# Kernel optimization log

Measured on AMD Instinct MI355X. Metric: run time of the kernel, lower is better.

## Reference

```python
import jax, jax.numpy as jnp
import numpy as np

B, C_IN, C_OUT, M, K1, K2 = 8, 256, 256, 4096, 4, 4


def _cheb_assemble(K, L, x):
    # x: (B, C_in, M) -> X: (B, C_in, M, K) with X[..., k] = L^k x
    # Batched as a single (M, M) @ (M, B*C_in) GEMM per power step.
    Bv, Cv, Mv = x.shape
    x0 = x.reshape(Bv * Cv, Mv).T  # (M, B*C_in)

    def step(carry, _):
        return L @ carry, carry  # emit L^k x, carry becomes L^{k+1} x

    _, ys = jax.lax.scan(step, x0, None, length=K)  # (K, M, B*C_in)
    return ys.transpose(2, 1, 0).reshape(Bv, Cv, Mv, K)


def setup_inputs() -> dict:
    key = jax.random.key(0)
    k1, k2, k3, k4 = jax.random.split(key, 4)
    scale = 1.0 / np.sqrt(M)  # keep spectral radius O(1) so L^k stays finite
    Ll = jax.random.normal(k1, (M, M), dtype=jnp.float32) * scale
    Lu = jax.random.normal(k2, (M, M), dtype=jnp.float32) * scale
    x = jax.random.normal(k3, (B, C_IN, M), dtype=jnp.float32)
    theta1 = jax.random.normal(k4, (C_OUT, C_IN, K1 + K2), dtype=jnp.float32)  # variance=1.0
    bias1 = jnp.zeros((1, C_OUT, 1), dtype=jnp.float32)
    return {"Ll": Ll, "Lu": Lu, "x": x, "theta1": theta1, "bias1": bias1}


def reference(Ll, Lu, x, theta1, bias1):
    X1 = _cheb_assemble(K1, Ll, x)  # (B, C_in, M, K1)
    X2 = _cheb_assemble(K2, Lu, x)  # (B, C_in, M, K2)
    X = jnp.concatenate((X1, X2), axis=3)  # (B, C_in, M, K1+K2)
    y = jnp.einsum("bimk,oik->bom", X, theta1)
    return y + bias1  # (B, C_out, M)
```

## Files before the change

kernel.cpp:

```cpp
#include <hip/hip_runtime.h>
#include <hip/hip_bf16.h>

typedef __hip_bfloat16 bf16;
typedef __attribute__((ext_vector_type(8))) short bshort8;
typedef __attribute__((ext_vector_type(4))) float f32x4;

#define GLL16(gsrc, ldst)                                                      \
  __builtin_amdgcn_global_load_lds(                                            \
      (const __attribute__((address_space(1))) void*)(gsrc),                   \
      (__attribute__((address_space(3))) void*)(ldst), 16, 0, 0)

#define MEMFENCE asm volatile("" ::: "memory")
#define BARRIER                                                                \
  do {                                                                         \
    MEMFENCE;                                                                  \
    __builtin_amdgcn_s_barrier();                                              \
    MEMFENCE;                                                                  \
  } while (0)
#define WAIT_LGKM0 asm volatile("s_waitcnt lgkmcnt(0)" ::: "memory")
#define WAIT_VM4 asm volatile("s_waitcnt vmcnt(4)" ::: "memory")

__global__ __launch_bounds__(256) void cast_f32_bf16(const float* __restrict__ src,
                                                     bf16* __restrict__ dst, int n4) {
  int stride = gridDim.x * blockDim.x;
  const float4* s4 = reinterpret_cast<const float4*>(src);
  __hip_bfloat162* d2 = reinterpret_cast<__hip_bfloat162*>(dst);
  for (int i = blockIdx.x * blockDim.x + threadIdx.x; i < n4; i += stride) {
    float4 v = s4[i];
    d2[2 * i]     = __float22bfloat162_rn(make_float2(v.x, v.y));
    d2[2 * i + 1] = __float22bfloat162_rn(make_float2(v.z, v.w));
  }
}

__global__ __launch_bounds__(256) void transpose_cast_x(const float* __restrict__ x,
                                                        bf16* __restrict__ Xt) {
  __shared__ bf16 t[64][65];
  int b = blockIdx.z;
  int m0 = blockIdx.x * 64;
  int i0 = blockIdx.y * 64;
  int tx = threadIdx.x & 63;
  int ty = threadIdx.x >> 6;
  for (int ii = ty; ii < 64; ii += 4)
    t[ii][tx] = __float2bfloat16(x[(size_t)(b * 256 + i0 + ii) * 4096 + m0 + tx]);
  __syncthreads();
  for (int mm = ty; mm < 64; mm += 4)
    Xt[(size_t)(b * 4096 + m0 + mm) * 256 + i0 + tx] = t[tx][mm];
}

__global__ __launch_bounds__(256) void build_theta(const float* __restrict__ th,
                                                   bf16* __restrict__ Tall) {
  int idx = blockIdx.x * 256 + threadIdx.x;
  int s = idx >> 16;
  int oi = idx & 65535;
  float v;
  if (s == 0)      v = th[oi * 8 + 0] + th[oi * 8 + 4];
  else if (s <= 3) v = th[oi * 8 + s];
  else             v = th[oi * 8 + s + 1];
  Tall[idx] = __float2bfloat16(v);
}

template <int EPI>
__device__ __forceinline__ void gemm_bt_tile(
    const bf16* __restrict__ A, const bf16* __restrict__ Bm, int K,
    bf16* __restrict__ Cb) {
  __shared__ __align__(16) bf16 As[128 * 32];
  __shared__ __align__(16) bf16 Bs[128 * 32];
  const int tid = threadIdx.x;
  const int lane = tid & 63;
  const int w = tid >> 6;
  const int wr = w >> 1, wc = w & 1;

  const int srow = w * 32 + (lane >> 2);
  const int scol = (lane & 3) * 8;
  bf16* ldsA0 = &As[(w * 32 + 0) * 32];
  bf16* ldsA1 = &As[(w * 32 + 16) * 32];
  bf16* ldsB0 = &Bs[(w * 32 + 0) * 32];
  bf16* ldsB1 = &Bs[(w * 32 + 16) * 32];
  const bf16* aptr0 = A + (size_t)srow * K + scol;
  const bf16* aptr1 = A + (size_t)(srow + 16) * K + scol;
  const bf16* bptr0 = Bm + (size_t)srow * K + scol;
  const bf16* bptr1 = Bm + (size_t)(srow + 16) * K + scol;

  f32x4 acc[4][4];
#pragma unroll
  for (int i = 0; i < 4; ++i)
#pragma unroll
    for (int j = 0; j < 4; ++j) acc[i][j] = (f32x4){0.f, 0.f, 0.f, 0.f};

  const int rsel = lane & 15;
  const int ksel = (lane >> 4) * 8;

  for (int kt = 0; kt < K; kt += 32) {
    GLL16(aptr0 + kt, ldsA0);
    GLL16(aptr1 + kt, ldsA1);
    GLL16(bptr0 + kt, ldsB0);
    GLL16(bptr1 + kt, ldsB1);
    __syncthreads();
    bshort8 av[4], bv[4];
#pragma unroll
    for (int m = 0; m < 4; ++m)
      av[m] = *reinterpret_cast<const bshort8*>(&As[(wr * 64 + m * 16 + rsel) * 32 + ksel]);
#pragma unroll
    for (int n = 0; n < 4; ++n)
      bv[n] = *reinterpret_cast<const bshort8*>(&Bs[(wc * 64 + n * 16 + rsel) * 32 + ksel]);
#pragma unroll
    for (int m = 0; m < 4; ++m)
#pragma unroll
      for (int n = 0; n < 4; ++n)
        acc[m][n] = __builtin_amdgcn_mfma_f32_16x16x32_bf16(av[m], bv[n], acc[m][n], 0, 0, 0);
    __syncthreads();
  }

  const int colf = lane & 15;
  const int rowf = (lane >> 4) * 4;
#pragma unroll
  for (int m = 0; m < 4; ++m) {
#pragma unroll
    for (int n = 0; n < 4; ++n) {
      int r0 = wr * 64 + m * 16 + rowf;
      int c = wc * 64 + n * 16 + colf;
#pragma unroll
      for (int r = 0; r < 4; ++r) {
        float v = acc[m][n][r];
        size_t off = (size_t)(r0 + r) * 4096 + c;
        Cb[off] = __float2bfloat16(v);
      }
    }
  }
}

__global__ __launch_bounds__(256) void chan_gemm(const bf16* __restrict__ Tall,
                                                 const bf16* __restrict__ Xt,
                                                 bf16* __restrict__ Vdst,
                                                 int slotL, int slotU) {
  int rt = blockIdx.x;
  int ct = blockIdx.y;
  int z = blockIdx.z;
  int chain = z >> 3, b = z & 7;
  int slot = chain ? slotU : slotL;
  const bf16* A = Tall + (size_t)slot * 65536 + (size_t)rt * 128 * 256;
  const bf16* Bm = Xt + (size_t)b * 4096 * 256 + (size_t)ct * 128 * 256;
  bf16* C = Vdst + ((size_t)z * 256 + rt * 128) * 4096 + ct * 128;
  gemm_bt_tile<0>(A, Bm, 256, C);
}

template <int EPI>
__global__ __launch_bounds__(512, 2) void gemm256(
    const bf16* __restrict__ Aall, const bf16* __restrict__ B0m,
    const bf16* __restrict__ B1m, bf16* __restrict__ Cb, float* __restrict__ Cf,
    const bf16* __restrict__ Db, int K) {
  const int tid = threadIdx.x;
  const int lane = tid & 63;
  const int w = tid >> 6;
  const int wr = w >> 2, wc = w & 3;

  int bid = blockIdx.x;
  int gid = (bid & 7) * 32 + (bid >> 3);
  const int rt = gid >> 4, ct = gid & 15;

  const bf16* Atile = Aall + (size_t)rt * 256 * K;
  const bf16* Btile = ((rt < 8) ? B0m : B1m) + (size_t)ct * 256 * K;

  __shared__ __align__(16) char lds_[131072];

  const int srow = tid >> 3;
  const int scol = (((tid & 7) ^ ((tid >> 3) & 7)) << 3);
  const bf16* gA = Atile + (size_t)srow * K + scol;
  const bf16* gB = Btile + (size_t)srow * K + scol;

#define STAGE_A(buf, half, kt)                                                 \
  do {                                                                         \
    char* l = &lds_[(buf)*65536 + (half)*16384 + w * 1024];                    \
    const bf16* g = gA + (size_t)((half)*128) * K + (size_t)(kt)*64;           \
    GLL16(g, l);                                                               \
    GLL16(g + (size_t)64 * K, l + 8192);                                       \
  } while (0)
#define STAGE_B(buf, half, kt)                                                 \
  do {                                                                         \
    char* l = &lds_[(buf)*65536 + 32768 + (half)*16384 + w * 1024];            \
    const bf16* g = gB + (size_t)((half)*128) * K + (size_t)(kt)*64;           \
    GLL16(g, l);                                                               \
    GLL16(g + (size_t)64 * K, l + 8192);                                       \
  } while (0)

  const int rsel = lane & 15;
  const int cbb = lane >> 4;
  const int xorv = rsel & 7;
  const int aBase = wr * 16384 + rsel * 128;
  const int bBase = 32768 + (wc >> 1) * 16384 + ((wc & 1) * 64 + rsel) * 128;
#define LDA(buf, mf, ks)                                                       \
  (*(const bshort8*)&lds_[(buf)*65536 + aBase + (mf)*2048 +                    \
                          (((((ks)*4) + cbb) ^ xorv) << 4)])
#define LDB(buf, nf, ks)                                                       \
  (*(const bshort8*)&lds_[(buf)*65536 + bBase + (nf)*2048 +                    \
                          (((((ks)*4) + cbb) ^ xorv) << 4)])

  f32x4 acc[8][4];
#pragma unroll
  for (int i = 0; i < 8; ++i)
#pragma unroll
    for (int j = 0; j < 4; ++j) acc[i][j] = (f32x4){0.f, 0.f, 0.f, 0.f};

  const int NT = K >> 6;
  const int NI = NT >> 1;

  bshort8 bfr[4][2];
  bshort8 afr[2][2];

#define MFMA16(Q)                                                              \
  do {                                                                         \
    _Pragma("unroll") for (int mi = 0; mi < 2; ++mi)                           \
    _Pragma("unroll") for (int nf = 0; nf < 4; ++nf)                           \
    _Pragma("unroll") for (int ks = 0; ks < 2; ++ks)                           \
        acc[(Q)*2 + mi][nf] = __builtin_amdgcn_mfma_f32_16x16x32_bf16(         \
            afr[mi][ks], bfr[nf][ks], acc[(Q)*2 + mi][nf], 0, 0, 0);           \
  } while (0)

#define PHASE(BUF, Q, STAGE_STMT, TAILWAIT)                                    \
  do {                                                                         \
    if ((Q) == 0) {                                                            \
      _Pragma("unroll") for (int nf = 0; nf < 4; ++nf)                         \
      _Pragma("unroll") for (int ks = 0; ks < 2; ++ks)                         \
          bfr[nf][ks] = LDB(BUF, nf, ks);                                      \
    }                                                                          \
    _Pragma("unroll") for (int mi = 0; mi < 2; ++mi)                           \
    _Pragma("unroll") for (int ks = 0; ks < 2; ++ks)                           \
        afr[mi][ks] = LDA(BUF, (Q)*2 + mi, ks);                                \
    STAGE_STMT;                                                                \
    BARRIER;                                                                   \
    WAIT_LGKM0;                                                                \
    __builtin_amdgcn_s_setprio(1);                                             \
    MFMA16(Q);                                                                 \
    __builtin_amdgcn_s_setprio(0);                                             \
    TAILWAIT;                                                                  \
    BARRIER;                                                                   \
  } while (0)

  STAGE_B(0, 0, 0); STAGE_B(0, 1, 0);
  STAGE_A(0, 0, 0); STAGE_A(0, 1, 0);
  STAGE_B(1, 0, 1); STAGE_B(1, 1, 1);
  WAIT_VM4;
  BARRIER;

  for (int it = 0; it < NI; ++it) {
    const int t1 = 2 * it + 1, t2 = 2 * it + 2, t3 = 2 * it + 3;
    const bool p2 = t2 < NT, p3 = t3 < NT;
    PHASE(0, 0, { STAGE_A(1, 0, t1); STAGE_A(1, 1, t1); }, {});
    PHASE(0, 1, { if (p2) STAGE_B(0, 0, t2); }, {});
    PHASE(0, 2, { if (p2) STAGE_B(0, 1, t2); }, {});
    PHASE(0, 3, {}, { WAIT_VM4; });
    PHASE(1, 0, { if (p2) STAGE_A(0, 0, t2); }, {});
    PHASE(1, 1, { if (p2) STAGE_A(0, 1, t2); }, {});
    PHASE(1, 2, { if (p3) STAGE_B(1, 0, t3); }, {});
    PHASE(1, 3, { if (p3) STAGE_B(1, 1, t3); }, { WAIT_VM4; });
  }

  const int colf = lane & 15;
  const int rowf = (lane >> 4) * 4;
  const size_t crow0 = (size_t)rt * 256 + wr * 128;
  const size_t ccol0 = (size_t)ct * 256 + wc * 64;
#pragma unroll
  for (int mf = 0; mf < 8; ++mf) {
#pragma unroll
    for (int nf = 0; nf < 4; ++nf) {
#pragma unroll
      for (int r = 0; r < 4; ++r) {
        size_t row = crow0 + mf * 16 + rowf + r;
        size_t col = ccol0 + nf * 16 + colf;
        size_t off = row * 4096 + col;
        float v = acc[mf][nf][r];
        if constexpr (EPI == 0) {
          v += __bfloat162float(Db[off]);
          Cb[off] = __float2bfloat16(v);
        } else {
          Cf[off] = v;
        }
      }
    }
  }
#undef STAGE_A
#undef STAGE_B
#undef LDA
#undef LDB
#undef MFMA16
#undef PHASE
}

__global__ __launch_bounds__(256) void reduce_final(const float* __restrict__ P,
                                                    const bf16* __restrict__ U0,
                                                    const float* __restrict__ bias,
                                                    float* __restrict__ Y) {
  const float4* P0 = (const float4*)P;
  const float4* P1 = (const float4*)(P + (size_t)2048 * 4096);
  float4* Y4 = (float4*)Y;
  const int n4 = 2048 * 4096 / 4;
  int stride = gridDim.x * blockDim.x;
  for (int i = blockIdx.x * 256 + threadIdx.x; i < n4; i += stride) {
    float4 a = P0[i];
    float4 b = P1[i];
    const ushort* u = (const ushort*)U0 + (size_t)i * 4;
    int r = (i >> 10);
    float bs = bias[r & 255];
    float4 o;
    o.x = a.x + b.x + __uint_as_float(((unsigned)u[0]) << 16) + bs;
    o.y = a.y + b.y + __uint_as_float(((unsigned)u[1]) << 16) + bs;
    o.z = a.z + b.z + __uint_as_float(((unsigned)u[2]) << 16) + bs;
    o.w = a.w + b.w + __uint_as_float(((unsigned)u[3]) << 16) + bs;
    Y4[i] = o;
  }
}

extern "C" void kernel_launch(void* const* d_in, const int* in_sizes, int n_in,
                              void* d_out, int out_size, void* d_ws, size_t ws_size,
                              hipStream_t stream) {
  const float* Ll = (const float*)d_in[0];
  const float* Lu = (const float*)d_in[1];
  const float* x = (const float*)d_in[2];
  const float* th = (const float*)d_in[3];
  const float* bias = (const float*)d_in[4];
  float* Y = (float*)d_out;

  char* ws = (char*)d_ws;
  const size_t SZ_L = (size_t)4096 * 4096 * 2;
  const size_t SZ_V = (size_t)2 * 8 * 256 * 4096 * 2;
  const size_t SZ_X = (size_t)8 * 4096 * 256 * 2;
  const size_t SZ_T = ((size_t)7 * 256 * 256 * 2 + 255) & ~(size_t)255;
  bf16* Llb = (bf16*)ws;  ws += SZ_L;
  bf16* Lub = (bf16*)ws;  ws += SZ_L;
  bf16* Xt  = (bf16*)ws;  ws += SZ_X;
  bf16* Tall = (bf16*)ws; ws += SZ_T;
  bf16* Vcur = (bf16*)ws; ws += SZ_V;
  bf16* Vnxt = (bf16*)ws; ws += SZ_V;
  bf16* Ustk = (bf16*)ws; ws += SZ_V;
  float* P = (float*)ws;  ws += (size_t)4096 * 4096 * 4;
  (void)ws_size; (void)in_sizes; (void)n_in; (void)out_size;

  cast_f32_bf16<<<2048, 256, 0, stream>>>(Ll, Llb, 4096 * 4096 / 4);
  cast_f32_bf16<<<2048, 256, 0, stream>>>(Lu, Lub, 4096 * 4096 / 4);
  transpose_cast_x<<<dim3(64, 4, 8), 256, 0, stream>>>(x, Xt);
  build_theta<<<1792, 256, 0, stream>>>(th, Tall);

  dim3 chanGrid(2, 32, 16);
  chan_gemm<<<chanGrid, 256, 0, stream>>>(Tall, Xt, Vcur, 3, 6);
  chan_gemm<<<chanGrid, 256, 0, stream>>>(Tall, Xt, Ustk, 2, 5);
  gemm256<0><<<256, 512, 0, stream>>>(Vcur, Llb, Lub, Vnxt, nullptr, Ustk, 4096);
  chan_gemm<<<chanGrid, 256, 0, stream>>>(Tall, Xt, Ustk, 1, 4);
  gemm256<0><<<256, 512, 0, stream>>>(Vnxt, Llb, Lub, Vcur, nullptr, Ustk, 4096);
  chan_gemm<<<dim3(2, 32, 8), 256, 0, stream>>>(Tall, Xt, Ustk, 0, 0);
  gemm256<1><<<256, 512, 0, stream>>>(Vcur, Llb, Lub, nullptr, P, nullptr, 4096);
  reduce_final<<<2048, 256, 0, stream>>>(P, Ustk, bias, Y);
}
```

Measured before the change: 493.7 us.

## Batch channel GEMMs into one launch, double-buffer LDS fragment reads, fuse epilogue

All channel-mixing GEMMs now run in a single launch that writes into separate U buffers, replacing four launches. The main 256-tile GEMM loop double-buffers its A/B register fragments so the LDS reads for the next phase are issued before the current MFMAs, hiding LDS latency. Its final epilogue folds in the U0 and bias additions for the first half of the output, leaving a simpler reduce that adds only the second partial. This adds register pressure and reworks the wait/barrier ordering, which could break correctness or occupancy.

```diff
diff --git a/kernel.cpp b/kernel.cpp
--- a/kernel.cpp
+++ b/kernel.cpp
@@ -18,7 +18,7 @@
     MEMFENCE;                                                                  \
   } while (0)
 #define WAIT_LGKM0 asm volatile("s_waitcnt lgkmcnt(0)" ::: "memory")
-#define WAIT_VM4 asm volatile("s_waitcnt vmcnt(4)" ::: "memory")
+#define WAIT_VM(n) asm volatile("s_waitcnt vmcnt(" #n ")" ::: "memory")
 
 __global__ __launch_bounds__(256) void cast_f32_bf16(const float* __restrict__ src,
                                                      bf16* __restrict__ dst, int n4) {
@@ -59,10 +59,9 @@
   Tall[idx] = __float2bfloat16(v);
 }
 
-template <int EPI>
-__device__ __forceinline__ void gemm_bt_tile(
-    const bf16* __restrict__ A, const bf16* __restrict__ Bm, int K,
-    bf16* __restrict__ Cb) {
+__device__ __forceinline__ void gemm_bt_tile(const bf16* __restrict__ A,
+                                             const bf16* __restrict__ Bm, int K,
+                                             bf16* __restrict__ Cb) {
   __shared__ __align__(16) bf16 As[128 * 32];
   __shared__ __align__(16) bf16 Bs[128 * 32];
   const int tid = threadIdx.x;
@@ -121,34 +120,51 @@
       int c = wc * 64 + n * 16 + colf;
 #pragma unroll
       for (int r = 0; r < 4; ++r) {
-        float v = acc[m][n][r];
         size_t off = (size_t)(r0 + r) * 4096 + c;
-        Cb[off] = __float2bfloat16(v);
+        Cb[off] = __float2bfloat16(acc[m][n][r]);
       }
     }
   }
 }
 
-__global__ __launch_bounds__(256) void chan_gemm(const bf16* __restrict__ Tall,
-                                                 const bf16* __restrict__ Xt,
-                                                 bf16* __restrict__ Vdst,
-                                                 int slotL, int slotU) {
+__global__ __launch_bounds__(256) void chan_all(const bf16* __restrict__ Tall,
+                                                const bf16* __restrict__ Xt,
+                                                bf16* __restrict__ U0,
+                                                bf16* __restrict__ U1,
+                                                bf16* __restrict__ U2,
+                                                bf16* __restrict__ U3) {
   int rt = blockIdx.x;
   int ct = blockIdx.y;
   int z = blockIdx.z;
-  int chain = z >> 3, b = z & 7;
-  int slot = chain ? slotU : slotL;
+  int slot, b;
+  bf16* Ubuf;
+  size_t rowbase;
+  if (z < 48) {
+    int k = 1 + z / 16;
+    int r = z % 16;
+    int chain = r >> 3;
+    b = r & 7;
+    slot = chain ? k + 3 : k;
+    Ubuf = (k == 1) ? U1 : ((k == 2) ? U2 : U3);
+    rowbase = (size_t)(chain * 2048 + b * 256);
+  } else {
+    b = z - 48;
+    slot = 0;
+    Ubuf = U0;
+    rowbase = (size_t)b * 256;
+  }
   const bf16* A = Tall + (size_t)slot * 65536 + (size_t)rt * 128 * 256;
   const bf16* Bm = Xt + (size_t)b * 4096 * 256 + (size_t)ct * 128 * 256;
-  bf16* C = Vdst + ((size_t)z * 256 + rt * 128) * 4096 + ct * 128;
-  gemm_bt_tile<0>(A, Bm, 256, C);
+  bf16* dst = Ubuf + (rowbase + (size_t)rt * 128) * 4096 + ct * 128;
+  gemm_bt_tile(A, Bm, 256, dst);
 }
 
 template <int EPI>
 __global__ __launch_bounds__(512, 2) void gemm256(
     const bf16* __restrict__ Aall, const bf16* __restrict__ B0m,
     const bf16* __restrict__ B1m, bf16* __restrict__ Cb, float* __restrict__ Cf,
-    const bf16* __restrict__ Db, int K) {
+    float* __restrict__ Cf2, const bf16* __restrict__ Db,
+    const float* __restrict__ bias, int K) {
   const int tid = threadIdx.x;
   const int lane = tid & 63;
   const int w = tid >> 6;
@@ -204,55 +220,69 @@
   const int NT = K >> 6;
   const int NI = NT >> 1;
 
-  bshort8 bfr[4][2];
-  bshort8 afr[2][2];
-
-#define MFMA16(Q)                                                              \
+  bshort8 afr0[2][2], afr1[2][2];
+  bshort8 bfr0[4][2], bfr1[4][2];
+
+#define RD_A(DST, BUF, Q)                                                      \
+  do {                                                                         \
+    DST[0][0] = LDA(BUF, (Q)*2 + 0, 0);                                        \
+    DST[0][1] = LDA(BUF, (Q)*2 + 0, 1);                                        \
+    DST[1][0] = LDA(BUF, (Q)*2 + 1, 0);                                        \
+    DST[1][1] = LDA(BUF, (Q)*2 + 1, 1);                                        \
+  } while (0)
+#define RD_B(DST, BUF)                                                         \
+  do {                                                                         \
+    DST[0][0] = LDB(BUF, 0, 0); DST[0][1] = LDB(BUF, 0, 1);                    \
+    DST[1][0] = LDB(BUF, 1, 0); DST[1][1] = LDB(BUF, 1, 1);                    \
+    DST[2][0] = LDB(BUF, 2, 0); DST[2][1] = LDB(BUF, 2, 1);                    \
+    DST[3][0] = LDB(BUF, 3, 0); DST[3][1] = LDB(BUF, 3, 1);                    \
+  } while (0)
+
+#define MFMA16(Q, AF, BF)                                                      \
   do {                                                                         \
     _Pragma("unroll") for (int mi = 0; mi < 2; ++mi)                           \
     _Pragma("unroll") for (int nf = 0; nf < 4; ++nf)                           \
     _Pragma("unroll") for (int ks = 0; ks < 2; ++ks)                           \
         acc[(Q)*2 + mi][nf] = __builtin_amdgcn_mfma_f32_16x16x32_bf16(         \
-            afr[mi][ks], bfr[nf][ks], acc[(Q)*2 + mi][nf], 0, 0, 0);           \
-  } while (0)
-
-#define PHASE(BUF, Q, STAGE_STMT, TAILWAIT)                                    \
-  do {                                                                         \
-    if ((Q) == 0) {                                                            \
-      _Pragma("unroll") for (int nf = 0; nf < 4; ++nf)                         \
-      _Pragma("unroll") for (int ks = 0; ks < 2; ++ks)                         \
-          bfr[nf][ks] = LDB(BUF, nf, ks);                                      \
-    }                                                                          \
-    _Pragma("unroll") for (int mi = 0; mi < 2; ++mi)                           \
-    _Pragma("unroll") for (int ks = 0; ks < 2; ++ks)                           \
-        afr[mi][ks] = LDA(BUF, (Q)*2 + mi, ks);                                \
-    STAGE_STMT;                                                                \
+            AF[mi][ks], BF[nf][ks], acc[(Q)*2 + mi][nf], 0, 0, 0);             \
+  } while (0)
+
+#define PHASE_(Q, AF, BF, RDSTMT, STAGESTMT, TAILSTMT)                         \
+  do {                                                                         \
+    WAIT_LGKM0;                                                                \
+    RDSTMT;                                                                    \
+    STAGESTMT;                                                                 \
     BARRIER;                                                                   \
-    WAIT_LGKM0;                                                                \
     __builtin_amdgcn_s_setprio(1);                                             \
-    MFMA16(Q);                                                                 \
+    MFMA16(Q, AF, BF);                                                         \
     __builtin_amdgcn_s_setprio(0);                                             \
-    TAILWAIT;                                                                  \
+    TAILSTMT;                                                                  \
     BARRIER;                                                                   \
   } while (0)
 
+  STAGE_A(0, 0, 0); STAGE_A(0, 1, 0);
   STAGE_B(0, 0, 0); STAGE_B(0, 1, 0);
-  STAGE_A(0, 0, 0); STAGE_A(0, 1, 0);
   STAGE_B(1, 0, 1); STAGE_B(1, 1, 1);
-  WAIT_VM4;
+  WAIT_VM(4);
   BARRIER;
+  RD_B(bfr0, 0);
+  RD_A(afr0, 0, 0);
 
   for (int it = 0; it < NI; ++it) {
     const int t1 = 2 * it + 1, t2 = 2 * it + 2, t3 = 2 * it + 3;
-    const bool p2 = t2 < NT, p3 = t3 < NT;
-    PHASE(0, 0, { STAGE_A(1, 0, t1); STAGE_A(1, 1, t1); }, {});
-    PHASE(0, 1, { if (p2) STAGE_B(0, 0, t2); }, {});
-    PHASE(0, 2, { if (p2) STAGE_B(0, 1, t2); }, {});
-    PHASE(0, 3, {}, { WAIT_VM4; });
-    PHASE(1, 0, { if (p2) STAGE_A(0, 0, t2); }, {});
-    PHASE(1, 1, { if (p2) STAGE_A(0, 1, t2); }, {});
-    PHASE(1, 2, { if (p3) STAGE_B(1, 0, t3); }, {});
-    PHASE(1, 3, { if (p3) STAGE_B(1, 1, t3); }, { WAIT_VM4; });
+    const bool p2v = t2 < NT, p3v = t3 < NT, last = (it == NI - 1);
+    PHASE_(0, afr0, bfr0, RD_A(afr1, 0, 1),
+           { STAGE_A(1, 0, t1); STAGE_A(1, 1, t1); }, {});
+    PHASE_(1, afr1, bfr0, RD_A(afr0, 0, 2), { if (p2v) STAGE_B(0, 0, t2); }, {});
+    PHASE_(2, afr0, bfr0, RD_A(afr1, 0, 3), { if (p2v) STAGE_B(0, 1, t2); },
+           { if (last) { WAIT_VM(0); } else { WAIT_VM(4); } });
+    PHASE_(3, afr1, bfr0, { RD_B(bfr1, 1); RD_A(afr0, 1, 0); }, {}, {});
+    PHASE_(0, afr0, bfr1, RD_A(afr1, 1, 1), { if (p2v) STAGE_A(0, 0, t2); }, {});
+    PHASE_(1, afr1, bfr1, RD_A(afr0, 1, 2), { if (p2v) STAGE_A(0, 1, t2); }, {});
+    PHASE_(2, afr0, bfr1, RD_A(afr1, 1, 3), { if (p3v) STAGE_B(1, 0, t3); },
+           { WAIT_VM(2); });
+    PHASE_(3, afr1, bfr1, { if (!last) { RD_B(bfr0, 0); RD_A(afr0, 0, 0); } },
+           { if (p3v) STAGE_B(1, 1, t3); }, {});
   }
 
   const int colf = lane & 15;
@@ -273,7 +303,12 @@
           v += __bfloat162float(Db[off]);
           Cb[off] = __float2bfloat16(v);
         } else {
-          Cf[off] = v;
+          if (rt < 8) {
+            v += __bfloat162float(Db[off]) + bias[row & 255];
+            Cf[off] = v;
+          } else {
+            Cf2[(row - 2048) * 4096 + col] = v;
+          }
         }
       }
     }
@@ -282,31 +317,23 @@
 #undef STAGE_B
 #undef LDA
 #undef LDB
+#undef RD_A
+#undef RD_B
 #undef MFMA16
-#undef PHASE
-}
-
-__global__ __launch_bounds__(256) void reduce_final(const float* __restrict__ P,
-                                                    const bf16* __restrict__ U0,
-                                                    const float* __restrict__ bias,
-                                                    float* __restrict__ Y) {
-  const float4* P0 = (const float4*)P;
-  const float4* P1 = (const float4*)(P + (size_t)2048 * 4096);
+#undef PHASE_
+}
+
+__global__ __launch_bounds__(256) void reduce_add(float* __restrict__ Y,
+                                                  const float* __restrict__ P1) {
   float4* Y4 = (float4*)Y;
+  const float4* P4 = (const float4*)P1;
   const int n4 = 2048 * 4096 / 4;
   int stride = gridDim.x * blockDim.x;
   for (int i = blockIdx.x * 256 + threadIdx.x; i < n4; i += stride) {
-    float4 a = P0[i];
-    float4 b = P1[i];
-    const ushort* u = (const ushort*)U0 + (size_t)i * 4;
-    int r = (i >> 10);
-    float bs = bias[r & 255];
-    float4 o;
-    o.x = a.x + b.x + __uint_as_float(((unsigned)u[0]) << 16) + bs;
-    o.y = a.y + b.y + __uint_as_float(((unsigned)u[1]) << 16) + bs;
-    o.z = a.z + b.z + __uint_as_float(((unsigned)u[2]) << 16) + bs;
-    o.w = a.w + b.w + __uint_as_float(((unsigned)u[3]) << 16) + bs;
-    Y4[i] = o;
+    float4 a = Y4[i];
+    float4 b = P4[i];
+    a.x += b.x; a.y += b.y; a.z += b.z; a.w += b.w;
+    Y4[i] = a;
   }
 }
 
@@ -322,17 +349,20 @@
 
   char* ws = (char*)d_ws;
   const size_t SZ_L = (size_t)4096 * 4096 * 2;
-  const size_t SZ_V = (size_t)2 * 8 * 256 * 4096 * 2;
+  const size_t SZ_U = (size_t)4096 * 4096 * 2;
   const size_t SZ_X = (size_t)8 * 4096 * 256 * 2;
   const size_t SZ_T = ((size_t)7 * 256 * 256 * 2 + 255) & ~(size_t)255;
-  bf16* Llb = (bf16*)ws;  ws += SZ_L;
-  bf16* Lub = (bf16*)ws;  ws += SZ_L;
-  bf16* Xt  = (bf16*)ws;  ws += SZ_X;
+  const size_t SZ_U0 = (size_t)2048 * 4096 * 2;
+  bf16* Llb = (bf16*)ws; ws += SZ_L;
+  bf16* Lub = (bf16*)ws; ws += SZ_L;
+  bf16* Xt  = (bf16*)ws; ws += SZ_X;
   bf16* Tall = (bf16*)ws; ws += SZ_T;
-  bf16* Vcur = (bf16*)ws; ws += SZ_V;
-  bf16* Vnxt = (bf16*)ws; ws += SZ_V;
-  bf16* Ustk = (bf16*)ws; ws += SZ_V;
-  float* P = (float*)ws;  ws += (size_t)4096 * 4096 * 4;
+  bf16* U1 = (bf16*)ws; ws += SZ_U;
+  bf16* U2 = (bf16*)ws; ws += SZ_U;
+  bf16* U3 = (bf16*)ws; ws += SZ_U;
+  bf16* U0 = (bf16*)ws; ws += SZ_U0;
+  bf16* V1 = (bf16*)ws; ws += SZ_U;
+  float* P1 = (float*)V1;
   (void)ws_size; (void)in_sizes; (void)n_in; (void)out_size;
 
   cast_f32_bf16<<<2048, 256, 0, stream>>>(Ll, Llb, 4096 * 4096 / 4);
@@ -340,13 +370,13 @@
   transpose_cast_x<<<dim3(64, 4, 8), 256, 0, stream>>>(x, Xt);
   build_theta<<<1792, 256, 0, stream>>>(th, Tall);
 
-  dim3 chanGrid(2, 32, 16);
-  chan_gemm<<<chanGrid, 256, 0, stream>>>(Tall, Xt, Vcur, 3, 6);
-  chan_gemm<<<chanGrid, 256, 0, stream>>>(Tall, Xt, Ustk, 2, 5);
-  gemm256<0><<<256, 512, 0, stream>>>(Vcur, Llb, Lub, Vnxt, nullptr, Ustk, 4096);
-  chan_gemm<<<chanGrid, 256, 0, stream>>>(Tall, Xt, Ustk, 1, 4);
-  gemm256<0><<<256, 512, 0, stream>>>(Vnxt, Llb, Lub, Vcur, nullptr, Ustk, 4096);
-  chan_gemm<<<dim3(2, 32, 8), 256, 0, stream>>>(Tall, Xt, Ustk, 0, 0);
-  gemm256<1><<<256, 512, 0, stream>>>(Vcur, Llb, Lub, nullptr, P, nullptr, 4096);
-  reduce_final<<<2048, 256, 0, stream>>>(P, Ustk, bias, Y);
-}
+  chan_all<<<dim3(2, 32, 56), 256, 0, stream>>>(Tall, Xt, U0, U1, U2, U3);
+
+  gemm256<0><<<256, 512, 0, stream>>>(U3, Llb, Lub, V1, nullptr, nullptr, U2,
+                                      nullptr, 4096);
+  gemm256<0><<<256, 512, 0, stream>>>(V1, Llb, Lub, U3, nullptr, nullptr, U1,
+                                      nullptr, 4096);
+  gemm256<2><<<256, 512, 0, stream>>>(U3, Llb, Lub, nullptr, Y, P1, U0, bias,
+                                      4096);
+  reduce_add<<<2048, 256, 0, stream>>>(Y, P1);
+}
```

New measurement: 709.2 us. +43.6%, slower.
